# Performance work log

Hardware: AMD Instinct MI355X
Metric: run time of the kernel (lower is better)

## Reference

```python
import jax, jax.numpy as jnp
import numpy as np

N_NODES, N_EDGES, F_IN, H1, H2, N_CLASSES = 10000, 640000, 128, 64, 32, 16


def gcn_conv(x, W, b, src, dst, n_nodes):
    """PyG GCNConv: x' = D^{-1/2} (A + I) D^{-1/2} (x W) + b, deg from dst + self-loop."""
    h = x @ W  # [N, out]
    deg = jax.ops.segment_sum(jnp.ones(src.shape[0], h.dtype), dst,
                              num_segments=n_nodes) + 1.0  # +1 self-loop
    dinv = jax.lax.rsqrt(deg)  # [N]
    coef = dinv[src] * dinv[dst]  # [E]
    agg = jax.ops.segment_sum(h[src] * coef[:, None], dst, num_segments=n_nodes)
    agg = agg + h * (dinv * dinv)[:, None]  # self-loop contribution
    return agg + b


def setup_inputs() -> dict:
    key = jax.random.key(0)
    ks = jax.random.split(key, 8)
    x = jax.random.normal(ks[0], (N_NODES, F_IN), jnp.float32)
    edge_index = jax.random.randint(ks[1], (2, N_EDGES), 0, N_NODES, jnp.int32)
    W1 = jax.random.normal(ks[2], (F_IN, H1), jnp.float32) / np.sqrt(F_IN)
    b1 = jnp.zeros((H1,), jnp.float32)
    W2 = jax.random.normal(ks[3], (H1, H2), jnp.float32) / np.sqrt(H1)
    b2 = jnp.zeros((H2,), jnp.float32)
    Wfc = jax.random.normal(ks[4], (H2, N_CLASSES), jnp.float32) / np.sqrt(H2)
    bfc = jnp.zeros((N_CLASSES,), jnp.float32)
    return {"x": x, "W1": W1, "b1": b1, "W2": W2, "b2": b2,
            "Wfc": Wfc, "bfc": bfc, "edge_index": edge_index}


def reference(x, W1, b1, W2, b2, Wfc, bfc, edge_index):
    src, dst = edge_index[0], edge_index[1]
    n = x.shape[0]
    h = jax.nn.relu(gcn_conv(x, W1, b1, src, dst, n))
    # dropout p=0.5 is identity in eval mode
    h = jax.nn.relu(gcn_conv(h, W2, b2, src, dst, n))
    g = jnp.mean(h, axis=0)  # [H2]
    return g @ Wfc + bfc  # [num_classes]
```

## Files before the change

kernel.cpp:

```cpp
#include <hip/hip_runtime.h>
#include <hip/hip_bf16.h>

#define N_NODES 10000
#define N_EDGES 640000
#define F_IN 128
#define H1 64
#define H2 32
#define N_CLASSES 16

#define NB 128
#define NPB 79
#define STAGE_C 64
#define SLOT 6144

__device__ __forceinline__ float bf_lo(unsigned u) {
    u <<= 16; float f; __builtin_memcpy(&f, &u, 4); return f;
}
__device__ __forceinline__ float bf_hi(unsigned u) {
    u &= 0xffff0000u; float f; __builtin_memcpy(&f, &u, 4); return f;
}

__global__ void __launch_bounds__(256) k_part(const int* __restrict__ src,
                                              const int* __restrict__ dst,
                                              int* __restrict__ bucketCursor,
                                              int* __restrict__ partBuf) {
    __shared__ int cnt[NB];
    __shared__ int gbase[NB];
    __shared__ int stage[NB * STAGE_C];
    int t = threadIdx.x;
    if (t < NB) cnt[t] = 0;
    __syncthreads();
    const int4* src4 = (const int4*)src;
    const int4* dst4 = (const int4*)dst;
#pragma unroll
    for (int k = 0; k < 2; ++k) {
        int i4 = blockIdx.x * 512 + k * 256 + t;
        if (i4 < N_EDGES / 4) {
            int4 s = src4[i4];
            int4 d = dst4[i4];
            int b, l, p;
            b = d.x / NPB; l = d.x - b * NPB; p = atomicAdd(&cnt[b], 1); stage[b * STAGE_C + p] = s.x | (l << 14);
            b = d.y / NPB; l = d.y - b * NPB; p = atomicAdd(&cnt[b], 1); stage[b * STAGE_C + p] = s.y | (l << 14);
            b = d.z / NPB; l = d.z - b * NPB; p = atomicAdd(&cnt[b], 1); stage[b * STAGE_C + p] = s.z | (l << 14);
            b = d.w / NPB; l = d.w - b * NPB; p = atomicAdd(&cnt[b], 1); stage[b * STAGE_C + p] = s.w | (l << 14);
        }
    }
    __syncthreads();
    if (t < NB) gbase[t] = atomicAdd(&bucketCursor[t], cnt[t]);
    __syncthreads();
    for (int i = t; i < NB * STAGE_C; i += 256) {
        int b = i >> 6;
        int k = i & (STAGE_C - 1);
        if (k < cnt[b]) partBuf[b * SLOT + gbase[b] + k] = stage[i];
    }
}

__global__ void __launch_bounds__(512) k_bsort(const int* __restrict__ bucketCursor,
                                               const int* __restrict__ partBuf,
                                               int* __restrict__ srcSorted,
                                               int* __restrict__ rowStart,
                                               float* __restrict__ dinv) {
    __shared__ int sc[NB];
    __shared__ int ldeg[NPB];
    __shared__ int lpre[NPB];
    __shared__ int cur[NPB];
    int t = threadIdx.x;
    int b = blockIdx.x;
    if (b == 0 && t == 0) rowStart[N_NODES] = N_EDGES;
    if (t < NB) sc[t] = bucketCursor[t];
    __syncthreads();
    for (int off = 1; off < NB; off <<= 1) {
        int v = (t >= off && t < NB) ? sc[t - off] : 0;
        __syncthreads();
        if (t < NB) sc[t] += v;
        __syncthreads();
    }
    int cnt = bucketCursor[b];
    int base = sc[b] - cnt;
    int nodeBase = b * NPB;
    int nNodes = N_NODES - nodeBase;
    if (nNodes <= 0) return;
    if (nNodes > NPB) nNodes = NPB;
    if (t < NPB) ldeg[t] = 0;
    __syncthreads();
    for (int i = t; i < cnt; i += 512) {
        int p = partBuf[b * SLOT + i];
        atomicAdd(&ldeg[p >> 14], 1);
    }
    __syncthreads();
    if (t == 0) {
        int run = 0;
        for (int i = 0; i < nNodes; ++i) { lpre[i] = run; run += ldeg[i]; }
    }
    __syncthreads();
    if (t < nNodes) {
        int v = nodeBase + t;
        rowStart[v] = base + lpre[t];
        cur[t] = lpre[t];
        dinv[v] = rsqrtf((float)ldeg[t] + 1.0f);
    }
    __syncthreads();
    for (int i = t; i < cnt; i += 512) {
        int p = partBuf[b * SLOT + i];
        int pos = atomicAdd(&cur[p >> 14], 1);
        srcSorted[base + pos] = p & 16383;
    }
}

__global__ void __launch_bounds__(256) k_gemm1(const float* __restrict__ x,
                                               const float* __restrict__ W1,
                                               const float* __restrict__ dinv,
                                               __hip_bfloat16* __restrict__ h1b) {
    __shared__ __align__(16) float w1s[F_IN][H1];
    __shared__ __align__(16) float xs[16][F_IN];
    int t = threadIdx.x;
    int node0 = blockIdx.x * 16;
    const float4* W14 = (const float4*)W1;
    float4* w1s4 = (float4*)w1s;
#pragma unroll
    for (int i = 0; i < 8; ++i) w1s4[i * 256 + t] = W14[i * 256 + t];
    const float4* x4 = (const float4*)(x + (long)node0 * F_IN);
    float4* xs4 = (float4*)xs;
#pragma unroll
    for (int i = 0; i < 2; ++i) xs4[i * 256 + t] = x4[i * 256 + t];
    __syncthreads();
    int j = t & 63;
    int q = t >> 6;
    int r0 = q * 4;
    float acc0 = 0.f, acc1 = 0.f, acc2 = 0.f, acc3 = 0.f;
#pragma unroll 4
    for (int k = 0; k < F_IN; ++k) {
        float w = w1s[k][j];
        acc0 += xs[r0 + 0][k] * w;
        acc1 += xs[r0 + 1][k] * w;
        acc2 += xs[r0 + 2][k] * w;
        acc3 += xs[r0 + 3][k] * w;
    }
    int v0 = node0 + r0;
    h1b[(v0 + 0) * H1 + j] = __float2bfloat16(acc0 * dinv[v0 + 0]);
    h1b[(v0 + 1) * H1 + j] = __float2bfloat16(acc1 * dinv[v0 + 1]);
    h1b[(v0 + 2) * H1 + j] = __float2bfloat16(acc2 * dinv[v0 + 2]);
    h1b[(v0 + 3) * H1 + j] = __float2bfloat16(acc3 * dinv[v0 + 3]);
}

__global__ void __launch_bounds__(256) k_gather1_gemm2(const __hip_bfloat16* __restrict__ h1b,
                                const int* __restrict__ rowStart,
                                const int* __restrict__ srcSorted,
                                const float* __restrict__ dinv,
                                const float* __restrict__ b1,
                                const float* __restrict__ W2,
                                __hip_bfloat16* __restrict__ h2b) {
    __shared__ float h1s[8][H1];
    int t = threadIdx.x;
    int n  = t >> 5;
    int fp = t & 31;
    int j0 = fp * 2;
    int v = blockIdx.x * 8 + n;
    float dv_ = dinv[v];
    int rs = rowStart[v], re = rowStart[v + 1];
    const unsigned* h1u = (const unsigned*)h1b;
    unsigned su = h1u[v * 32 + fp];
    float fx = bf_lo(su), fy = bf_hi(su);
    float x0 = 0.f, y0 = 0.f, x1 = 0.f, y1 = 0.f;
    float x2 = 0.f, y2 = 0.f, x3 = 0.f, y3 = 0.f;
    int e = rs;
    for (; e + 4 <= re; e += 4) {
        int i0 = srcSorted[e],     i1 = srcSorted[e + 1];
        int i2 = srcSorted[e + 2], i3 = srcSorted[e + 3];
        unsigned u0 = h1u[i0 * 32 + fp];
        unsigned u1 = h1u[i1 * 32 + fp];
        unsigned u2 = h1u[i2 * 32 + fp];
        unsigned u3 = h1u[i3 * 32 + fp];
        x0 += bf_lo(u0); y0 += bf_hi(u0);
        x1 += bf_lo(u1); y1 += bf_hi(u1);
        x2 += bf_lo(u2); y2 += bf_hi(u2);
        x3 += bf_lo(u3); y3 += bf_hi(u3);
    }
    for (; e < re; ++e) {
        unsigned u = h1u[srcSorted[e] * 32 + fp];
        fx += bf_lo(u); fy += bf_hi(u);
    }
    fx += (x0 + x1) + (x2 + x3);
    fy += (y0 + y1) + (y2 + y3);
    h1s[n][j0]     = fmaxf(dv_ * fx + b1[j0], 0.f);
    h1s[n][j0 + 1] = fmaxf(dv_ * fy + b1[j0 + 1], 0.f);
    __syncthreads();
    float acc = 0.f;
#pragma unroll
    for (int kk = 0; kk < H1; ++kk)
        acc += h1s[n][kk] * W2[kk * H2 + fp];
    h2b[v * H2 + fp] = __float2bfloat16(acc * dv_);
}

__global__ void __launch_bounds__(256) k_gather2_mean(const __hip_bfloat16* __restrict__ h2b,
                               const int* __restrict__ rowStart,
                               const int* __restrict__ srcSorted,
                               const float* __restrict__ dinv,
                               const float* __restrict__ b2,
                               float* __restrict__ g) {
    __shared__ float red[16][H2];
    int t = threadIdx.x;
    int n  = t >> 4;
    int fp = t & 15;
    int j0 = fp * 2;
    int v = blockIdx.x * 16 + n;
    float dv_ = dinv[v];
    int rs = rowStart[v], re = rowStart[v + 1];
    const unsigned* h2u = (const unsigned*)h2b;
    unsigned su = h2u[v * 16 + fp];
    float fx = bf_lo(su), fy = bf_hi(su);
    float x0 = 0.f, y0 = 0.f, x1 = 0.f, y1 = 0.f;
    float x2 = 0.f, y2 = 0.f, x3 = 0.f, y3 = 0.f;
    int e = rs;
    for (; e + 4 <= re; e += 4) {
        int i0 = srcSorted[e],     i1 = srcSorted[e + 1];
        int i2 = srcSorted[e + 2], i3 = srcSorted[e + 3];
        unsigned u0 = h2u[i0 * 16 + fp];
        unsigned u1 = h2u[i1 * 16 + fp];
        unsigned u2 = h2u[i2 * 16 + fp];
        unsigned u3 = h2u[i3 * 16 + fp];
        x0 += bf_lo(u0); y0 += bf_hi(u0);
        x1 += bf_lo(u1); y1 += bf_hi(u1);
        x2 += bf_lo(u2); y2 += bf_hi(u2);
        x3 += bf_lo(u3); y3 += bf_hi(u3);
    }
    for (; e < re; ++e) {
        unsigned u = h2u[srcSorted[e] * 16 + fp];
        fx += bf_lo(u); fy += bf_hi(u);
    }
    fx += (x0 + x1) + (x2 + x3);
    fy += (y0 + y1) + (y2 + y3);
    red[n][j0]     = fmaxf(dv_ * fx + b2[j0], 0.f);
    red[n][j0 + 1] = fmaxf(dv_ * fy + b2[j0 + 1], 0.f);
    __syncthreads();
    if (t < 32) {
        float s = 0.f;
#pragma unroll
        for (int r = 0; r < 16; ++r) s += red[r][t];
        atomicAdd(&g[t], s);
    }
}

__global__ void k_out(const float* __restrict__ g,
                      const float* __restrict__ Wfc,
                      const float* __restrict__ bfc,
                      float* __restrict__ out) {
    int c = threadIdx.x;
    if (c < N_CLASSES) {
        float acc = 0.f;
#pragma unroll
        for (int j = 0; j < H2; ++j)
            acc += g[j] * Wfc[j * N_CLASSES + c];
        float invN = 1.0f / (float)N_NODES;
        out[c] = acc * invN + bfc[c];
    }
}

extern "C" void kernel_launch(void* const* d_in, const int* in_sizes, int n_in,
                              void* d_out, int out_size, void* d_ws, size_t ws_size,
                              hipStream_t stream) {
    const float* x   = (const float*)d_in[0];
    const float* W1  = (const float*)d_in[1];
    const float* b1  = (const float*)d_in[2];
    const float* W2  = (const float*)d_in[3];
    const float* b2  = (const float*)d_in[4];
    const float* Wfc = (const float*)d_in[5];
    const float* bfc = (const float*)d_in[6];
    const int* edge = (const int*)d_in[7];
    const int* srcI = edge;
    const int* dstI = edge + N_EDGES;
    float* out = (float*)d_out;

    char* ws = (char*)d_ws;
    int*   bucketCursor = (int*)  (ws + 0);
    float* g            = (float*)(ws + 512);
    float* dinv         = (float*)(ws + 1024);
    int*   rowStart     = (int*)  (ws + 41984);
    int*   srcSorted    = (int*)  (ws + 82944);
    int*   partBuf      = (int*)  (ws + 2643968);
    __hip_bfloat16* h1b = (__hip_bfloat16*)(ws + 2643968);
    __hip_bfloat16* h2b = (__hip_bfloat16*)(ws + 3923968);

    hipMemsetAsync(bucketCursor, 0, 640, stream);

    k_part<<<(N_EDGES / 4 + 511) / 512, 256, 0, stream>>>(srcI, dstI, bucketCursor, partBuf);
    k_bsort<<<NB, 512, 0, stream>>>(bucketCursor, partBuf, srcSorted, rowStart, dinv);
    k_gemm1<<<N_NODES / 16, 256, 0, stream>>>(x, W1, dinv, h1b);
    k_gather1_gemm2<<<N_NODES / 8, 256, 0, stream>>>(h1b, rowStart, srcSorted,
                                                     dinv, b1, W2, h2b);
    k_gather2_mean<<<N_NODES / 16, 256, 0, stream>>>(h2b, rowStart, srcSorted,
                                                     dinv, b2, g);
    k_out<<<1, 64, 0, stream>>>(g, Wfc, bfc, out);
}
```

Before: 136.7 us.

## Store sorted sources as ushort, stage per-block indices in LDS, fuse output

Sorted source indices are stored as 16-bit values, halving index traffic. Both gather kernels cooperatively stage the block's contiguous index range into LDS before gathering, which replaces per-lane redundant global index loads with LDS reads, and fall back to global loads if the range exceeds 4096 entries. The final classifier kernel is folded into the second gather kernel through a last-block-done counter, removing one launch. The cost is extra syncs, LDS footprint that may lower occupancy, and a threadfence plus atomic per block.

Result: slower. 160.1 us (+17.1%).

```diff
diff --git a/kernel.cpp b/kernel.cpp
--- a/kernel.cpp
+++ b/kernel.cpp
@@ -12,6 +12,9 @@
 #define NPB 79
 #define STAGE_C 64
 #define SLOT 6144
+#define IDX_CAP 4096
+
+typedef unsigned short ushortT;
 
 __device__ __forceinline__ float bf_lo(unsigned u) {
     u <<= 16; float f; __builtin_memcpy(&f, &u, 4); return f;
@@ -57,7 +60,7 @@
 
 __global__ void __launch_bounds__(512) k_bsort(const int* __restrict__ bucketCursor,
                                                const int* __restrict__ partBuf,
-                                               int* __restrict__ srcSorted,
+                                               ushortT* __restrict__ srcU,
                                                int* __restrict__ rowStart,
                                                float* __restrict__ dinv) {
     __shared__ int sc[NB];
@@ -103,7 +106,7 @@
     for (int i = t; i < cnt; i += 512) {
         int p = partBuf[b * SLOT + i];
         int pos = atomicAdd(&cur[p >> 14], 1);
-        srcSorted[base + pos] = p & 16383;
+        srcU[base + pos] = (ushortT)(p & 16383);
     }
 }
 
@@ -145,17 +148,24 @@
 
 __global__ void __launch_bounds__(256) k_gather1_gemm2(const __hip_bfloat16* __restrict__ h1b,
                                 const int* __restrict__ rowStart,
-                                const int* __restrict__ srcSorted,
+                                const ushortT* __restrict__ srcU,
                                 const float* __restrict__ dinv,
                                 const float* __restrict__ b1,
                                 const float* __restrict__ W2,
                                 __hip_bfloat16* __restrict__ h2b) {
     __shared__ float h1s[8][H1];
+    __shared__ ushortT idxs[IDX_CAP];
+    __shared__ int sRange[2];
     int t = threadIdx.x;
     int n  = t >> 5;
     int fp = t & 31;
-    int j0 = fp * 2;
     int v = blockIdx.x * 8 + n;
+    if (t == 0) { sRange[0] = rowStart[blockIdx.x * 8]; sRange[1] = rowStart[blockIdx.x * 8 + 8]; }
+    __syncthreads();
+    int rs0 = sRange[0];
+    int cnt0 = sRange[1] - rs0;
+    bool useLds = (cnt0 <= IDX_CAP);
+    if (useLds) for (int i = t; i < cnt0; i += 256) idxs[i] = srcU[rs0 + i];
     float dv_ = dinv[v];
     int rs = rowStart[v], re = rowStart[v + 1];
     const unsigned* h1u = (const unsigned*)h1b;
@@ -163,27 +173,35 @@
     float fx = bf_lo(su), fy = bf_hi(su);
     float x0 = 0.f, y0 = 0.f, x1 = 0.f, y1 = 0.f;
     float x2 = 0.f, y2 = 0.f, x3 = 0.f, y3 = 0.f;
-    int e = rs;
-    for (; e + 4 <= re; e += 4) {
-        int i0 = srcSorted[e],     i1 = srcSorted[e + 1];
-        int i2 = srcSorted[e + 2], i3 = srcSorted[e + 3];
-        unsigned u0 = h1u[i0 * 32 + fp];
-        unsigned u1 = h1u[i1 * 32 + fp];
-        unsigned u2 = h1u[i2 * 32 + fp];
-        unsigned u3 = h1u[i3 * 32 + fp];
-        x0 += bf_lo(u0); y0 += bf_hi(u0);
-        x1 += bf_lo(u1); y1 += bf_hi(u1);
-        x2 += bf_lo(u2); y2 += bf_hi(u2);
-        x3 += bf_lo(u3); y3 += bf_hi(u3);
-    }
-    for (; e < re; ++e) {
-        unsigned u = h1u[srcSorted[e] * 32 + fp];
-        fx += bf_lo(u); fy += bf_hi(u);
+    __syncthreads();
+    if (useLds) {
+        int le = rs - rs0, lend = re - rs0;
+        for (; le + 4 <= lend; le += 4) {
+            int i0 = idxs[le],     i1 = idxs[le + 1];
+            int i2 = idxs[le + 2], i3 = idxs[le + 3];
+            unsigned u0 = h1u[i0 * 32 + fp];
+            unsigned u1 = h1u[i1 * 32 + fp];
+            unsigned u2 = h1u[i2 * 32 + fp];
+            unsigned u3 = h1u[i3 * 32 + fp];
+            x0 += bf_lo(u0); y0 += bf_hi(u0);
+            x1 += bf_lo(u1); y1 += bf_hi(u1);
+            x2 += bf_lo(u2); y2 += bf_hi(u2);
+            x3 += bf_lo(u3); y3 += bf_hi(u3);
+        }
+        for (; le < lend; ++le) {
+            unsigned u = h1u[idxs[le] * 32 + fp];
+            fx += bf_lo(u); fy += bf_hi(u);
+        }
+    } else {
+        for (int e = rs; e < re; ++e) {
+            unsigned u = h1u[(int)srcU[e] * 32 + fp];
+            fx += bf_lo(u); fy += bf_hi(u);
+        }
     }
     fx += (x0 + x1) + (x2 + x3);
     fy += (y0 + y1) + (y2 + y3);
-    h1s[n][j0]     = fmaxf(dv_ * fx + b1[j0], 0.f);
-    h1s[n][j0 + 1] = fmaxf(dv_ * fy + b1[j0 + 1], 0.f);
+    ((float2*)h1s[n])[fp] = make_float2(fmaxf(dv_ * fx + b1[fp * 2], 0.f),
+                                        fmaxf(dv_ * fy + b1[fp * 2 + 1], 0.f));
     __syncthreads();
     float acc = 0.f;
 #pragma unroll
@@ -192,18 +210,31 @@
     h2b[v * H2 + fp] = __float2bfloat16(acc * dv_);
 }
 
-__global__ void __launch_bounds__(256) k_gather2_mean(const __hip_bfloat16* __restrict__ h2b,
+__global__ void __launch_bounds__(256) k_gather2_out(const __hip_bfloat16* __restrict__ h2b,
                                const int* __restrict__ rowStart,
-                               const int* __restrict__ srcSorted,
+                               const ushortT* __restrict__ srcU,
                                const float* __restrict__ dinv,
                                const float* __restrict__ b2,
-                               float* __restrict__ g) {
+                               float* __restrict__ g,
+                               int* __restrict__ doneCnt,
+                               const float* __restrict__ Wfc,
+                               const float* __restrict__ bfc,
+                               float* __restrict__ out) {
     __shared__ float red[16][H2];
+    __shared__ ushortT idxs[IDX_CAP];
+    __shared__ int sRange[2];
+    __shared__ int amLast;
+    __shared__ float gs[H2];
     int t = threadIdx.x;
     int n  = t >> 4;
     int fp = t & 15;
-    int j0 = fp * 2;
     int v = blockIdx.x * 16 + n;
+    if (t == 0) { sRange[0] = rowStart[blockIdx.x * 16]; sRange[1] = rowStart[blockIdx.x * 16 + 16]; }
+    __syncthreads();
+    int rs0 = sRange[0];
+    int cnt0 = sRange[1] - rs0;
+    bool useLds = (cnt0 <= IDX_CAP);
+    if (useLds) for (int i = t; i < cnt0; i += 256) idxs[i] = srcU[rs0 + i];
     float dv_ = dinv[v];
     int rs = rowStart[v], re = rowStart[v + 1];
     const unsigned* h2u = (const unsigned*)h2b;
@@ -211,48 +242,55 @@
     float fx = bf_lo(su), fy = bf_hi(su);
     float x0 = 0.f, y0 = 0.f, x1 = 0.f, y1 = 0.f;
     float x2 = 0.f, y2 = 0.f, x3 = 0.f, y3 = 0.f;
-    int e = rs;
-    for (; e + 4 <= re; e += 4) {
-        int i0 = srcSorted[e],     i1 = srcSorted[e + 1];
-        int i2 = srcSorted[e + 2], i3 = srcSorted[e + 3];
-        unsigned u0 = h2u[i0 * 16 + fp];
-        unsigned u1 = h2u[i1 * 16 + fp];
-        unsigned u2 = h2u[i2 * 16 + fp];
-        unsigned u3 = h2u[i3 * 16 + fp];
-        x0 += bf_lo(u0); y0 += bf_hi(u0);
-        x1 += bf_lo(u1); y1 += bf_hi(u1);
-        x2 += bf_lo(u2); y2 += bf_hi(u2);
-        x3 += bf_lo(u3); y3 += bf_hi(u3);
-    }
-    for (; e < re; ++e) {
-        unsigned u = h2u[srcSorted[e] * 16 + fp];
-        fx += bf_lo(u); fy += bf_hi(u);
+    __syncthreads();
+    if (useLds) {
+        int le = rs - rs0, lend = re - rs0;
+        for (; le + 4 <= lend; le += 4) {
+            int i0 = idxs[le],     i1 = idxs[le + 1];
+            int i2 = idxs[le + 2], i3 = idxs[le + 3];
+            unsigned u0 = h2u[i0 * 16 + fp];
+            unsigned u1 = h2u[i1 * 16 + fp];
+            unsigned u2 = h2u[i2 * 16 + fp];
+            unsigned u3 = h2u[i3 * 16 + fp];
+            x0 += bf_lo(u0); y0 += bf_hi(u0);
+            x1 += bf_lo(u1); y1 += bf_hi(u1);
+            x2 += bf_lo(u2); y2 += bf_hi(u2);
+            x3 += bf_lo(u3); y3 += bf_hi(u3);
+        }
+        for (; le < lend; ++le) {
+            unsigned u = h2u[idxs[le] * 16 + fp];
+            fx += bf_lo(u); fy += bf_hi(u);
+        }
+    } else {
+        for (int e = rs; e < re; ++e) {
+            unsigned u = h2u[(int)srcU[e] * 16 + fp];
+            fx += bf_lo(u); fy += bf_hi(u);
+        }
     }
     fx += (x0 + x1) + (x2 + x3);
     fy += (y0 + y1) + (y2 + y3);
-    red[n][j0]     = fmaxf(dv_ * fx + b2[j0], 0.f);
-    red[n][j0 + 1] = fmaxf(dv_ * fy + b2[j0 + 1], 0.f);
-    __syncthreads();
-    if (t < 32) {
+    ((float2*)red[n])[fp] = make_float2(fmaxf(dv_ * fx + b2[fp * 2], 0.f),
+                                        fmaxf(dv_ * fy + b2[fp * 2 + 1], 0.f));
+    __syncthreads();
+    if (t < H2) {
         float s = 0.f;
 #pragma unroll
         for (int r = 0; r < 16; ++r) s += red[r][t];
         atomicAdd(&g[t], s);
     }
-}
-
-__global__ void k_out(const float* __restrict__ g,
-                      const float* __restrict__ Wfc,
-                      const float* __restrict__ bfc,
-                      float* __restrict__ out) {
-    int c = threadIdx.x;
-    if (c < N_CLASSES) {
-        float acc = 0.f;
-#pragma unroll
-        for (int j = 0; j < H2; ++j)
-            acc += g[j] * Wfc[j * N_CLASSES + c];
-        float invN = 1.0f / (float)N_NODES;
-        out[c] = acc * invN + bfc[c];
+    __threadfence();
+    if (t == 0) amLast = (atomicAdd(doneCnt, 1) == (int)gridDim.x - 1);
+    __syncthreads();
+    if (amLast) {
+        if (t < H2) gs[t] = atomicAdd(&g[t], 0.f);
+        __syncthreads();
+        if (t < N_CLASSES) {
+            float acc = 0.f;
+#pragma unroll
+            for (int j = 0; j < H2; ++j)
+                acc += gs[j] * Wfc[j * N_CLASSES + t];
+            out[t] = acc * (1.0f / (float)N_NODES) + bfc[t];
+        }
     }
 }
 
@@ -272,23 +310,24 @@
     float* out = (float*)d_out;
 
     char* ws = (char*)d_ws;
-    int*   bucketCursor = (int*)  (ws + 0);
-    float* g            = (float*)(ws + 512);
-    float* dinv         = (float*)(ws + 1024);
-    int*   rowStart     = (int*)  (ws + 41984);
-    int*   srcSorted    = (int*)  (ws + 82944);
-    int*   partBuf      = (int*)  (ws + 2643968);
-    __hip_bfloat16* h1b = (__hip_bfloat16*)(ws + 2643968);
-    __hip_bfloat16* h2b = (__hip_bfloat16*)(ws + 3923968);
-
-    hipMemsetAsync(bucketCursor, 0, 640, stream);
+    int*     bucketCursor = (int*)    (ws + 0);
+    float*   g            = (float*)  (ws + 512);
+    int*     doneCnt      = (int*)    (ws + 640);
+    float*   dinv         = (float*)  (ws + 1024);
+    int*     rowStart     = (int*)    (ws + 41984);
+    ushortT* srcU         = (ushortT*)(ws + 82944);
+    int*     partBuf      = (int*)    (ws + 1363968);
+    __hip_bfloat16* h1b   = (__hip_bfloat16*)(ws + 1363968);
+    __hip_bfloat16* h2b   = (__hip_bfloat16*)(ws + 2643968);
+
+    hipMemsetAsync(bucketCursor, 0, 768, stream);
 
     k_part<<<(N_EDGES / 4 + 511) / 512, 256, 0, stream>>>(srcI, dstI, bucketCursor, partBuf);
-    k_bsort<<<NB, 512, 0, stream>>>(bucketCursor, partBuf, srcSorted, rowStart, dinv);
+    k_bsort<<<NB, 512, 0, stream>>>(bucketCursor, partBuf, srcU, rowStart, dinv);
     k_gemm1<<<N_NODES / 16, 256, 0, stream>>>(x, W1, dinv, h1b);
-    k_gather1_gemm2<<<N_NODES / 8, 256, 0, stream>>>(h1b, rowStart, srcSorted,
+    k_gather1_gemm2<<<N_NODES / 8, 256, 0, stream>>>(h1b, rowStart, srcU,
                                                      dinv, b1, W2, h2b);
-    k_gather2_mean<<<N_NODES / 16, 256, 0, stream>>>(h2b, rowStart, srcSorted,
-                                                     dinv, b2, g);
-    k_out<<<1, 64, 0, stream>>>(g, Wfc, bfc, out);
-}
+    k_gather2_out<<<N_NODES / 16, 256, 0, stream>>>(h2b, rowStart, srcU,
+                                                    dinv, b2, g, doneCnt,
+                                                    Wfc, bfc, out);
+}
```
